# Kernel optimization log

Hardware: AMD Instinct MI355X
Metric: run time of the kernel (lower is better)

## Reference

```python
import jax, jax.numpy as jnp
import numpy as np

B = 131072
SD, AD, HID = 24, 8, 32
NH = SD + AD            # n_heads = 32
UNITS = HID * NH        # 1024


def _xavier(k, shape):
    fan_in, fan_out = shape[-2], shape[-1]
    lim = float(np.sqrt(6.0 / (fan_in + fan_out)))
    return jax.random.uniform(k, shape, jnp.float32, -lim, lim)


def setup_inputs() -> dict:
    key = jax.random.key(0)
    ks = jax.random.split(key, 8)
    return dict(
        state=jax.random.normal(ks[0], (B, SD), jnp.float32),
        action=jax.random.normal(ks[1], (B, AD), jnp.float32),
        # ripple layer 1: per-head Linear(NH -> HID), gate logits init 0 (init_prob=0.5)
        W1=_xavier(ks[2], (NH, NH, HID)), b1=jnp.zeros((NH, HID), jnp.float32), g1=jnp.zeros((NH,), jnp.float32),
        # ripple layer 2: per-head Linear(UNITS -> HID)
        W2=_xavier(ks[3], (NH, UNITS, HID)), b2=jnp.zeros((NH, HID), jnp.float32), g2=jnp.zeros((NH,), jnp.float32),
        # q_network
        Wq1=_xavier(ks[4], (UNITS, 256)), bq1=jnp.zeros((256,), jnp.float32),
        ln1_g=jnp.ones((256,), jnp.float32), ln1_b=jnp.zeros((256,), jnp.float32),
        Wq2=_xavier(ks[5], (256, 128)), bq2=jnp.zeros((128,), jnp.float32),
        ln2_g=jnp.ones((128,), jnp.float32), ln2_b=jnp.zeros((128,), jnp.float32),
        Wq3=_xavier(ks[6], (128, 1)), bq3=jnp.zeros((1,), jnp.float32),
    )


def _ripple(x, W, b, g):
    # x: [B, D]; W: [H, D, K]; per-head linear + tanh, scaled by per-head sigmoid gate
    h = jnp.tanh(jnp.einsum('bd,hdk->bhk', x, W) + b[None])  # [B, H, K]
    h = h * jax.nn.sigmoid(g)[None, :, None]
    return h.reshape(x.shape[0], -1)  # [B, H*K]


def _ln(x, g, b, eps=1e-5):
    mu = jnp.mean(x, -1, keepdims=True)
    var = jnp.mean((x - mu) ** 2, -1, keepdims=True)
    return (x - mu) * jax.lax.rsqrt(var + eps) * g + b


def reference(state, action, W1, b1, g1, W2, b2, g2,
              Wq1, bq1, ln1_g, ln1_b, Wq2, bq2, ln2_g, ln2_b, Wq3, bq3):
    sa = jnp.concatenate([state, action], axis=1)          # [B, SD+AD]
    x = _ripple(sa, W1, b1, g1)                            # [B, UNITS]
    x = _ripple(x, W2, b2, g2)                             # [B, UNITS]
    h = jax.nn.relu(_ln(x @ Wq1 + bq1, ln1_g, ln1_b))      # [B, 256] (dropout = eval identity)
    h = jax.nn.relu(_ln(h @ Wq2 + bq2, ln2_g, ln2_b))      # [B, 128]
    return h @ Wq3 + bq3                                   # [B, 1]
```

## Files before the change

kernel.cpp:

```cpp
#include <hip/hip_runtime.h>
#include <hip/hip_bf16.h>

typedef _Float16 f16x8 __attribute__((ext_vector_type(8)));
typedef _Float16 f16x4 __attribute__((ext_vector_type(4)));
typedef float f32x4 __attribute__((ext_vector_type(4)));

__device__ __forceinline__ float tanh_fast(float x) {
  float e = __expf(2.0f * x);
  return 1.0f - 2.0f * __builtin_amdgcn_rcpf(e + 1.0f);
}
__device__ __forceinline__ float sigmoid_fast(float x) {
  return __builtin_amdgcn_rcpf(1.0f + __expf(-x));
}

__global__ __launch_bounds__(256) void prep_weights(
    const float* __restrict__ W1, const float* __restrict__ W2,
    const float* __restrict__ Wq1, const float* __restrict__ Wq2,
    _Float16* __restrict__ V1p, _Float16* __restrict__ V2p,
    _Float16* __restrict__ T1p, _Float16* __restrict__ T2p) {
  __shared__ float S[32 * 33];
  int b = blockIdx.x, t = threadIdx.x;
  if (b < 2624) {
    const float* in; _Float16* out; int N, nc0, tile, use_pi;
    if (b < 2048) {
      int h = b >> 6, rem = b & 63, ntl = rem >> 5, kt = rem & 31;
      in = W2 + (size_t)h * 32768 + (size_t)kt * 32 * 32;
      N = 32; nc0 = ntl * 16;
      out = V2p; tile = kt * 64 + (h * 2 + ntl); use_pi = 1;
    } else if (b < 2560) {
      int i = b - 2048, nt = i >> 5, kt = i & 31;
      in = Wq1 + (size_t)kt * 32 * 256; N = 256; nc0 = nt * 16;
      out = T1p; tile = kt * 16 + nt; use_pi = 1;
    } else {
      int i = b - 2560, nt = i >> 3, kt = i & 7;
      in = Wq2 + (size_t)kt * 32 * 128; N = 128; nc0 = nt * 16;
      out = T2p; tile = nt * 8 + kt; use_pi = 0;
    }
    if (t < 128) {
      int r = t >> 2, c4 = (t & 3) * 4;
      const float4 v = *(const float4*)(in + (size_t)r * N + nc0 + c4);
      S[r * 17 + c4 + 0] = v.x; S[r * 17 + c4 + 1] = v.y;
      S[r * 17 + c4 + 2] = v.z; S[r * 17 + c4 + 3] = v.w;
    }
    __syncthreads();
    if (t < 128) {
      int w2 = t >> 6, l = t & 63, q = l >> 4, l15 = l & 15;
      f16x4 o;
#pragma unroll
      for (int jj = 0; jj < 4; ++jj) {
        int kl = use_pi ? (q * 4 + jj + w2 * 16) : (q * 8 + w2 * 4 + jj);
        o[jj] = (_Float16)S[kl * 17 + l15];
      }
      *(f16x4*)(out + (size_t)tile * 512 + l * 8 + w2 * 4) = o;
    }
  } else {
    int h = b - 2624;
    const float* in = W1 + h * 1024;
    int cc = t & 31, rr8 = t >> 5;
#pragma unroll
    for (int p = 0; p < 4; ++p) {
      int r = rr8 + p * 8;
      S[cc * 33 + r] = in[r * 32 + cc];
    }
    __syncthreads();
    if (t < 128) {
      int ntl = t >> 6, l = t & 63, q = l >> 4, l15 = l & 15;
      f16x8 o;
#pragma unroll
      for (int j = 0; j < 8; ++j)
        o[j] = (_Float16)S[(ntl * 16 + l15) * 33 + q * 8 + j];
      *(f16x8*)(V1p + (size_t)(h * 2 + ntl) * 512 + l * 8) = o;
    }
  }
}

__global__ __launch_bounds__(256, 2) void k12_fused(
    const float* __restrict__ state, const float* __restrict__ action,
    const _Float16* __restrict__ v1p, const float* __restrict__ b1,
    const float* __restrict__ g1,
    const _Float16* __restrict__ v2p, const float* __restrict__ b2,
    const float* __restrict__ g2,
    _Float16* __restrict__ x2p, int gro, int NRT) {
  __shared__ __align__(16) _Float16 SA[128 * 40];
  __shared__ __align__(16) _Float16 XF[2 * 16384];
  int g = blockIdx.x;
  int bn2 = g & 3, bm = g >> 2;
  int t = threadIdx.x, w = t >> 6, l = t & 63, q = l >> 4, l15 = l & 15;
  int wrow = w & 1, cg2 = w >> 1;
  int m0 = bm * 128;

  {
    int r = t >> 1, half = t & 1;
    size_t grow = (size_t)(gro + m0 + r);
    float v[16];
    if (half == 0) {
      const float4* sp = (const float4*)(state + grow * 24);
      ((float4*)v)[0] = sp[0]; ((float4*)v)[1] = sp[1];
      ((float4*)v)[2] = sp[2]; ((float4*)v)[3] = sp[3];
    } else {
      const float4* sp = (const float4*)(state + grow * 24 + 16);
      ((float4*)v)[0] = sp[0]; ((float4*)v)[1] = sp[1];
      const float4* ap = (const float4*)(action + grow * 8);
      ((float4*)v)[2] = ap[0]; ((float4*)v)[3] = ap[1];
    }
    f16x8 h0, h1;
#pragma unroll
    for (int j = 0; j < 8; ++j) { h0[j] = (_Float16)v[j]; h1[j] = (_Float16)v[8 + j]; }
    *(f16x8*)&SA[r * 40 + half * 16] = h0;
    *(f16x8*)&SA[r * 40 + half * 16 + 8] = h1;
  }
  __syncthreads();

  f16x8 asa[4];
#pragma unroll
  for (int p = 0; p < 4; ++p)
    asa[p] = *(const f16x8*)&SA[((wrow * 4 + p) * 16 + l15) * 40 + q * 8];

  const int nt0 = bn2 * 16 + cg2 * 8;
  const _Float16* bBase = v2p + (size_t)nt0 * 512 + (size_t)l * 8;
  f32x4 acc[4][8] = {};

  auto Rphase = [&](int kcn) {
#pragma unroll
    for (int e = 0; e < 2; ++e) {
      f16x8 rb0 = *(const f16x8*)(v1p + (size_t)(kcn * 8 + cg2 * 4 + 2 * e) * 512 + l * 8);
      f16x8 rb1 = *(const f16x8*)(v1p + (size_t)(kcn * 8 + cg2 * 4 + 2 * e + 1) * 512 + l * 8);
      float sg = sigmoid_fast(g1[kcn * 4 + cg2 * 2 + e]);
      const float* bp = b1 + kcn * 128 + cg2 * 64 + e * 32 + q * 4;
      f32x4 bs0 = *(const f32x4*)(bp);
      f32x4 bs1 = *(const f32x4*)(bp + 16);
      _Float16* bw = XF + ((kcn & 1) * 16384);
#pragma unroll
      for (int p = 0; p < 4; ++p) {
        f32x4 d0 = {}, d1 = {};
        d0 = __builtin_amdgcn_mfma_f32_16x16x32_f16(rb0, asa[p], d0, 0, 0, 0);
        d1 = __builtin_amdgcn_mfma_f32_16x16x32_f16(rb1, asa[p], d1, 0, 0, 0);
        f16x8 o;
#pragma unroll
        for (int r = 0; r < 4; ++r) {
          o[r]     = (_Float16)(tanh_fast(d0[r] + bs0[r]) * sg);
          o[4 + r] = (_Float16)(tanh_fast(d1[r] + bs1[r]) * sg);
        }
        *(f16x8*)(bw + (size_t)((2 * cg2 + e) * 8 + wrow * 4 + p) * 512 + l * 8) = o;
      }
    }
  };

  f16x8 bb0[4], bb1v[4];
#pragma unroll
  for (int n2 = 0; n2 < 4; ++n2)
    bb0[n2] = *(const f16x8*)(bBase + (size_t)n2 * 512);
#pragma unroll
  for (int n2 = 0; n2 < 4; ++n2)
    bb1v[n2] = *(const f16x8*)(bBase + (size_t)(4 + n2) * 512);
  Rphase(0);
  __syncthreads();

#pragma unroll
  for (int kc = 0; kc < 8; ++kc) {
    const _Float16* buf = XF + ((kc & 1) * 16384);
#pragma unroll
    for (int j = 0; j < 4; ++j) {
      if (j == 2 && kc < 7) Rphase(kc + 1);
      int kt = kc * 4 + j;
      f16x8 xa[4];
#pragma unroll
      for (int mi = 0; mi < 4; ++mi)
        xa[mi] = *(const f16x8*)(buf + (size_t)(j * 8 + wrow * 4 + mi) * 512 + l * 8);
#pragma unroll
      for (int mi = 0; mi < 4; ++mi)
#pragma unroll
        for (int n2 = 0; n2 < 4; ++n2)
          acc[mi][n2] = __builtin_amdgcn_mfma_f32_16x16x32_f16(bb0[n2], xa[mi], acc[mi][n2], 0, 0, 0);
      if (kt < 31) {
#pragma unroll
        for (int n2 = 0; n2 < 4; ++n2)
          bb0[n2] = *(const f16x8*)(bBase + (size_t)((kt + 1) * 64 + n2) * 512);
      }
#pragma unroll
      for (int mi = 0; mi < 4; ++mi)
#pragma unroll
        for (int n2 = 0; n2 < 4; ++n2)
          acc[mi][4 + n2] = __builtin_amdgcn_mfma_f32_16x16x32_f16(bb1v[n2], xa[mi], acc[mi][4 + n2], 0, 0, 0);
      if (kt < 31) {
#pragma unroll
        for (int n2 = 0; n2 < 4; ++n2)
          bb1v[n2] = *(const f16x8*)(bBase + (size_t)((kt + 1) * 64 + 4 + n2) * 512);
      }
    }
    __syncthreads();
  }

#pragma unroll
  for (int mi = 0; mi < 4; ++mi) {
    int rt = bm * 8 + wrow * 4 + mi;
#pragma unroll
    for (int p2 = 0; p2 < 4; ++p2) {
      int kc2 = (nt0 >> 1) + p2;
      float sg2 = sigmoid_fast(g2[kc2]);
      f32x4 c0 = *(const f32x4*)(b2 + kc2 * 32 + q * 4);
      f32x4 c1 = *(const f32x4*)(b2 + kc2 * 32 + 16 + q * 4);
      f16x8 o;
#pragma unroll
      for (int r = 0; r < 4; ++r) {
        o[r]     = (_Float16)(tanh_fast(acc[mi][2 * p2][r] + c0[r]) * sg2);
        o[4 + r] = (_Float16)(tanh_fast(acc[mi][2 * p2 + 1][r] + c1[r]) * sg2);
      }
      *(f16x8*)(x2p + ((size_t)kc2 * NRT + rt) * 512 + l * 8) = o;
    }
  }
}

__global__ __launch_bounds__(512, 3) void k3_head(
    const _Float16* __restrict__ x2p, const _Float16* __restrict__ t1p,
    const _Float16* __restrict__ t2p,
    const float* __restrict__ bq1, const float* __restrict__ ln1g, const float* __restrict__ ln1b,
    const float* __restrict__ bq2, const float* __restrict__ ln2g, const float* __restrict__ ln2b,
    const float* __restrict__ wq3, const float* __restrict__ bq3,
    float* __restrict__ out, int NRT, int SROWS) {
  __shared__ __align__(16) _Float16 y1h[128 * 264];
  __shared__ float redA[128 * 4], redB[128 * 4];
  __shared__ float meanv[128], rstdv[128];
  int bm = blockIdx.x;
  int t = threadIdx.x, w = t >> 6, l = t & 63, q = l >> 4, l15 = l & 15;
  int wr = w >> 2, wc = w & 3;

  int gt = bm * 8;
  int slice = 0;
  if (gt >= NRT) { slice = 1; gt -= NRT; }
  int rt0 = gt + wr * 4;

  f32x4 acc[4][4] = {};
  const size_t aStep = (size_t)NRT * 512;
  const _Float16* aP = x2p + (size_t)slice * SROWS * 1024 + (size_t)rt0 * 512 + (size_t)l * 8;
  const _Float16* bP = t1p + (size_t)(wc * 4) * 512 + (size_t)l * 8;

  f16x8 a0[4], a1[4], b0[4], b1[4];
#pragma unroll
  for (int mi = 0; mi < 4; ++mi) a0[mi] = *(const f16x8*)(aP + mi * 512);
#pragma unroll
  for (int ni = 0; ni < 4; ++ni) b0[ni] = *(const f16x8*)(bP + ni * 512);
#pragma unroll
  for (int mi = 0; mi < 4; ++mi) a1[mi] = *(const f16x8*)(aP + aStep + mi * 512);
#pragma unroll
  for (int ni = 0; ni < 4; ++ni) b1[ni] = *(const f16x8*)(bP + 8192 + ni * 512);
  aP += 2 * aStep; bP += 16384;

  for (int kt = 0; kt < 32; kt += 2) {
#pragma unroll
    for (int mi = 0; mi < 4; ++mi)
#pragma unroll
      for (int ni = 0; ni < 4; ++ni)
        acc[mi][ni] = __builtin_amdgcn_mfma_f32_16x16x32_f16(a0[mi], b0[ni], acc[mi][ni], 0, 0, 0);
    if (kt < 30) {
#pragma unroll
      for (int mi = 0; mi < 4; ++mi) a0[mi] = *(const f16x8*)(aP + mi * 512);
#pragma unroll
      for (int ni = 0; ni < 4; ++ni) b0[ni] = *(const f16x8*)(bP + ni * 512);
    }
#pragma unroll
    for (int mi = 0; mi < 4; ++mi)
#pragma unroll
      for (int ni = 0; ni < 4; ++ni)
        acc[mi][ni] = __builtin_amdgcn_mfma_f32_16x16x32_f16(a1[mi], b1[ni], acc[mi][ni], 0, 0, 0);
    if (kt < 30) {
#pragma unroll
      for (int mi = 0; mi < 4; ++mi) a1[mi] = *(const f16x8*)(aP + aStep + mi * 512);
#pragma unroll
      for (int ni = 0; ni < 4; ++ni) b1[ni] = *(const f16x8*)(bP + 8192 + ni * 512);
      aP += 2 * aStep; bP += 16384;
    }
  }

#pragma unroll
  for (int ni = 0; ni < 4; ++ni) {
    int col = wc * 64 + ni * 16 + l15;
    float b = bq1[col];
#pragma unroll
    for (int mi = 0; mi < 4; ++mi)
#pragma unroll
      for (int r = 0; r < 4; ++r) acc[mi][ni][r] += b;
  }
#pragma unroll
  for (int mi = 0; mi < 4; ++mi)
#pragma unroll
    for (int r = 0; r < 4; ++r) {
      int row = wr * 64 + mi * 16 + q * 4 + r;
      float s = 0.f, sq = 0.f;
#pragma unroll
      for (int ni = 0; ni < 4; ++ni) { float v = acc[mi][ni][r]; s += v; sq += v * v; }
#pragma unroll
      for (int off = 1; off < 16; off <<= 1) { s += __shfl_xor(s, off); sq += __shfl_xor(sq, off); }
      if (l15 == 0) { redA[row * 4 + wc] = s; redB[row * 4 + wc] = sq; }
    }
  __syncthreads();
  if (t < 128) {
    float s  = redA[t * 4] + redA[t * 4 + 1] + redA[t * 4 + 2] + redA[t * 4 + 3];
    float sq = redB[t * 4] + redB[t * 4 + 1] + redB[t * 4 + 2] + redB[t * 4 + 3];
    float mean = s * (1.0f / 256.0f);
    float var = sq * (1.0f / 256.0f) - mean * mean;
    meanv[t] = mean; rstdv[t] = rsqrtf(var + 1e-5f);
  }
  __syncthreads();
#pragma unroll
  for (int mi = 0; mi < 4; ++mi)
#pragma unroll
    for (int ni = 0; ni < 4; ++ni)
#pragma unroll
      for (int r = 0; r < 4; ++r) {
        int row = wr * 64 + mi * 16 + q * 4 + r;
        int col = wc * 64 + ni * 16 + l15;
        float y = (acc[mi][ni][r] - meanv[row]) * rstdv[row] * ln1g[col] + ln1b[col];
        y = fmaxf(y, 0.f);
        y1h[row * 264 + col] = (_Float16)y;
      }
  __syncthreads();

  f32x4 a2[4][2] = {};
  for (int kt = 0; kt < 8; ++kt) {
    f16x8 af2[4];
#pragma unroll
    for (int mi = 0; mi < 4; ++mi)
      af2[mi] = *(const f16x8*)&y1h[(wr * 64 + mi * 16 + l15) * 264 + kt * 32 + q * 8];
#pragma unroll
    for (int ni = 0; ni < 2; ++ni) {
      f16x8 bf = *(const f16x8*)(t2p + (size_t)(wc * 2 + ni) * 4096 + kt * 512 + l * 8);
#pragma unroll
      for (int mi = 0; mi < 4; ++mi)
        a2[mi][ni] = __builtin_amdgcn_mfma_f32_16x16x32_f16(af2[mi], bf, a2[mi][ni], 0, 0, 0);
    }
  }
#pragma unroll
  for (int ni = 0; ni < 2; ++ni) {
    int col = wc * 32 + ni * 16 + l15;
    float b = bq2[col];
#pragma unroll
    for (int mi = 0; mi < 4; ++mi)
#pragma unroll
      for (int r = 0; r < 4; ++r) a2[mi][ni][r] += b;
  }
  __syncthreads();
#pragma unroll
  for (int mi = 0; mi < 4; ++mi)
#pragma unroll
    for (int r = 0; r < 4; ++r) {
      int row = wr * 64 + mi * 16 + q * 4 + r;
      float s = 0.f, sq = 0.f;
#pragma unroll
      for (int ni = 0; ni < 2; ++ni) { float v = a2[mi][ni][r]; s += v; sq += v * v; }
#pragma unroll
      for (int off = 1; off < 16; off <<= 1) { s += __shfl_xor(s, off); sq += __shfl_xor(sq, off); }
      if (l15 == 0) { redA[row * 4 + wc] = s; redB[row * 4 + wc] = sq; }
    }
  __syncthreads();
  if (t < 128) {
    float s  = redA[t * 4] + redA[t * 4 + 1] + redA[t * 4 + 2] + redA[t * 4 + 3];
    float sq = redB[t * 4] + redB[t * 4 + 1] + redB[t * 4 + 2] + redB[t * 4 + 3];
    float mean = s * (1.0f / 128.0f);
    float var = sq * (1.0f / 128.0f) - mean * mean;
    meanv[t] = mean; rstdv[t] = rsqrtf(var + 1e-5f);
  }
  __syncthreads();
#pragma unroll
  for (int mi = 0; mi < 4; ++mi)
#pragma unroll
    for (int r = 0; r < 4; ++r) {
      int row = wr * 64 + mi * 16 + q * 4 + r;
      float pr = 0.f;
#pragma unroll
      for (int ni = 0; ni < 2; ++ni) {
        int col = wc * 32 + ni * 16 + l15;
        float y = (a2[mi][ni][r] - meanv[row]) * rstdv[row] * ln2g[col] + ln2b[col];
        y = fmaxf(y, 0.f);
        pr += y * wq3[col];
      }
#pragma unroll
      for (int off = 1; off < 16; off <<= 1) pr += __shfl_xor(pr, off);
      if (l15 == 0) redA[row * 4 + wc] = pr;
    }
  __syncthreads();
  if (t < 128)
    out[bm * 128 + t] = redA[t * 4] + redA[t * 4 + 1] + redA[t * 4 + 2] + redA[t * 4 + 3] + bq3[0];
}

extern "C" void kernel_launch(void* const* d_in, const int* in_sizes, int n_in,
                              void* d_out, int out_size, void* d_ws, size_t ws_size,
                              hipStream_t stream) {
  const float* state  = (const float*)d_in[0];
  const float* action = (const float*)d_in[1];
  const float* W1  = (const float*)d_in[2];
  const float* b1  = (const float*)d_in[3];
  const float* g1  = (const float*)d_in[4];
  const float* W2  = (const float*)d_in[5];
  const float* b2  = (const float*)d_in[6];
  const float* g2  = (const float*)d_in[7];
  const float* Wq1 = (const float*)d_in[8];
  const float* bq1 = (const float*)d_in[9];
  const float* ln1g = (const float*)d_in[10];
  const float* ln1b = (const float*)d_in[11];
  const float* Wq2 = (const float*)d_in[12];
  const float* bq2 = (const float*)d_in[13];
  const float* ln2g = (const float*)d_in[14];
  const float* ln2b = (const float*)d_in[15];
  const float* Wq3 = (const float*)d_in[16];
  const float* bq3 = (const float*)d_in[17];
  int B = in_sizes[0] / 24;

  char* ws = (char*)d_ws;
  _Float16* V1p = (_Float16*)(ws);
  _Float16* V2p = (_Float16*)(ws + 65536);
  _Float16* T1p = (_Float16*)(ws + 65536 + 2097152);
  _Float16* T2p = (_Float16*)(ws + 65536 + 2097152 + 524288);
  size_t woff = (65536 + 2097152 + 524288 + 65536 + 4095) & ~(size_t)4095;

  size_t avail = ws_size > woff ? ws_size - woff : 0;
  long rows = (long)(avail / 2048);
  if (rows > 32768) rows = 32768;
  rows &= ~127L;
  if (rows < 128) rows = 128;
  int S = (int)rows;
  _Float16* x2 = (_Float16*)(ws + woff);
  int NRT = S / 16;

  prep_weights<<<2656, 256, 0, stream>>>(W1, W2, Wq1, Wq2, V1p, V2p, T1p, T2p);

  for (int r0 = 0; r0 < B; r0 += S) {
    int Sc = S < (B - r0) ? S : (B - r0);
    int nbm = Sc / 128;
    k12_fused<<<dim3(4 * nbm), 256, 0, stream>>>(state, action, V1p, b1, g1,
                                                 V2p, b2, g2, x2, r0, NRT);
    k3_head<<<dim3(Sc / 128), 512, 0, stream>>>(x2, T1p, T2p, bq1, ln1g, ln1b,
                                                bq2, ln2g, ln2b, Wq3, bq3,
                                                (float*)d_out + r0, NRT, S);
  }
}
```

Before: 622.2 us.

## Split fused ripple kernel into separate ripple1 and ripple2 kernels

The fused kernel that recomputed ripple layer 1 inside each column block is split in two. A standalone kernel writes layer-1 activations to global workspace, and a 512-thread ripple2 GEMM kernel streams them straight from global memory with a three-deep register prefetch, with no LDS and no per-chunk barriers. This removes the 4x redundant layer-1 recompute, the LDS double buffering and the syncs, but adds a global round trip for x1. It also halves the rows per chunk because workspace is now shared with x1.

```diff
diff --git a/kernel.cpp b/kernel.cpp
--- a/kernel.cpp
+++ b/kernel.cpp
@@ -74,121 +74,115 @@
   }
 }
 
-__global__ __launch_bounds__(256, 2) void k12_fused(
+__global__ __launch_bounds__(256) void k1_ripple1(
     const float* __restrict__ state, const float* __restrict__ action,
     const _Float16* __restrict__ v1p, const float* __restrict__ b1,
-    const float* __restrict__ g1,
-    const _Float16* __restrict__ v2p, const float* __restrict__ b2,
-    const float* __restrict__ g2,
-    _Float16* __restrict__ x2p, int gro, int NRT) {
-  __shared__ __align__(16) _Float16 SA[128 * 40];
-  __shared__ __align__(16) _Float16 XF[2 * 16384];
+    const float* __restrict__ g1, _Float16* __restrict__ x1p,
+    int gro, int NRT) {
+  __shared__ __align__(16) _Float16 SA[64 * 40];
+  int bm = blockIdx.x;
+  int t = threadIdx.x, w = t >> 6, l = t & 63, q = l >> 4, l15 = l & 15;
+  {
+    int r = t >> 2, qq = t & 3;
+    size_t grow = (size_t)(gro + bm * 64 + r);
+    const float* src = (qq < 3) ? (state + grow * 24 + qq * 8)
+                                : (action + grow * 8);
+    float4 v0 = ((const float4*)src)[0];
+    float4 v1 = ((const float4*)src)[1];
+    float v[8] = {v0.x, v0.y, v0.z, v0.w, v1.x, v1.y, v1.z, v1.w};
+    f16x8 h;
+#pragma unroll
+    for (int j = 0; j < 8; ++j) h[j] = (_Float16)v[j];
+    *(f16x8*)&SA[r * 40 + qq * 8] = h;
+  }
+  __syncthreads();
+
+  f16x8 asa[4];
+#pragma unroll
+  for (int p = 0; p < 4; ++p)
+    asa[p] = *(const f16x8*)&SA[(p * 16 + l15) * 40 + q * 8];
+
+#pragma unroll
+  for (int i = 0; i < 8; ++i) {
+    int ktL = w * 8 + i;
+    f16x8 rb0 = *(const f16x8*)(v1p + (size_t)(2 * ktL) * 512 + l * 8);
+    f16x8 rb1 = *(const f16x8*)(v1p + (size_t)(2 * ktL + 1) * 512 + l * 8);
+    float sg = sigmoid_fast(g1[ktL]);
+    f32x4 bs0 = *(const f32x4*)(b1 + ktL * 32 + q * 4);
+    f32x4 bs1 = *(const f32x4*)(b1 + ktL * 32 + 16 + q * 4);
+    _Float16* op = x1p + ((size_t)ktL * NRT + bm * 4) * 512 + l * 8;
+#pragma unroll
+    for (int p = 0; p < 4; ++p) {
+      f32x4 d0 = {}, d1 = {};
+      d0 = __builtin_amdgcn_mfma_f32_16x16x32_f16(rb0, asa[p], d0, 0, 0, 0);
+      d1 = __builtin_amdgcn_mfma_f32_16x16x32_f16(rb1, asa[p], d1, 0, 0, 0);
+      f16x8 o;
+#pragma unroll
+      for (int r = 0; r < 4; ++r) {
+        o[r]     = (_Float16)(tanh_fast(d0[r] + bs0[r]) * sg);
+        o[4 + r] = (_Float16)(tanh_fast(d1[r] + bs1[r]) * sg);
+      }
+      *(f16x8*)(op + (size_t)p * 512) = o;
+    }
+  }
+}
+
+__global__ __launch_bounds__(512, 2) void k2_ripple2(
+    const _Float16* __restrict__ x1p, const _Float16* __restrict__ v2p,
+    const float* __restrict__ b2, const float* __restrict__ g2,
+    _Float16* __restrict__ x2p, int NRT) {
   int g = blockIdx.x;
-  int bn2 = g & 3, bm = g >> 2;
+  int bn = g & 1, bm = g >> 1;
   int t = threadIdx.x, w = t >> 6, l = t & 63, q = l >> 4, l15 = l & 15;
-  int wrow = w & 1, cg2 = w >> 1;
-  int m0 = bm * 128;
-
-  {
-    int r = t >> 1, half = t & 1;
-    size_t grow = (size_t)(gro + m0 + r);
-    float v[16];
-    if (half == 0) {
-      const float4* sp = (const float4*)(state + grow * 24);
-      ((float4*)v)[0] = sp[0]; ((float4*)v)[1] = sp[1];
-      ((float4*)v)[2] = sp[2]; ((float4*)v)[3] = sp[3];
-    } else {
-      const float4* sp = (const float4*)(state + grow * 24 + 16);
-      ((float4*)v)[0] = sp[0]; ((float4*)v)[1] = sp[1];
-      const float4* ap = (const float4*)(action + grow * 8);
-      ((float4*)v)[2] = ap[0]; ((float4*)v)[3] = ap[1];
-    }
-    f16x8 h0, h1;
-#pragma unroll
-    for (int j = 0; j < 8; ++j) { h0[j] = (_Float16)v[j]; h1[j] = (_Float16)v[8 + j]; }
-    *(f16x8*)&SA[r * 40 + half * 16] = h0;
-    *(f16x8*)&SA[r * 40 + half * 16 + 8] = h1;
-  }
-  __syncthreads();
-
-  f16x8 asa[4];
-#pragma unroll
-  for (int p = 0; p < 4; ++p)
-    asa[p] = *(const f16x8*)&SA[((wrow * 4 + p) * 16 + l15) * 40 + q * 8];
-
-  const int nt0 = bn2 * 16 + cg2 * 8;
+  int wrow = w >> 2, wcol = w & 3;
+  const int nt0 = bn * 32 + wcol * 8;
   const _Float16* bBase = v2p + (size_t)nt0 * 512 + (size_t)l * 8;
+  const _Float16* aBase = x1p + (size_t)(bm * 8 + wrow * 4) * 512 + (size_t)l * 8;
+  const size_t aK = (size_t)NRT * 512;
+
   f32x4 acc[4][8] = {};
-
-  auto Rphase = [&](int kcn) {
-#pragma unroll
-    for (int e = 0; e < 2; ++e) {
-      f16x8 rb0 = *(const f16x8*)(v1p + (size_t)(kcn * 8 + cg2 * 4 + 2 * e) * 512 + l * 8);
-      f16x8 rb1 = *(const f16x8*)(v1p + (size_t)(kcn * 8 + cg2 * 4 + 2 * e + 1) * 512 + l * 8);
-      float sg = sigmoid_fast(g1[kcn * 4 + cg2 * 2 + e]);
-      const float* bp = b1 + kcn * 128 + cg2 * 64 + e * 32 + q * 4;
-      f32x4 bs0 = *(const f32x4*)(bp);
-      f32x4 bs1 = *(const f32x4*)(bp + 16);
-      _Float16* bw = XF + ((kcn & 1) * 16384);
-#pragma unroll
-      for (int p = 0; p < 4; ++p) {
-        f32x4 d0 = {}, d1 = {};
-        d0 = __builtin_amdgcn_mfma_f32_16x16x32_f16(rb0, asa[p], d0, 0, 0, 0);
-        d1 = __builtin_amdgcn_mfma_f32_16x16x32_f16(rb1, asa[p], d1, 0, 0, 0);
-        f16x8 o;
-#pragma unroll
-        for (int r = 0; r < 4; ++r) {
-          o[r]     = (_Float16)(tanh_fast(d0[r] + bs0[r]) * sg);
-          o[4 + r] = (_Float16)(tanh_fast(d1[r] + bs1[r]) * sg);
-        }
-        *(f16x8*)(bw + (size_t)((2 * cg2 + e) * 8 + wrow * 4 + p) * 512 + l * 8) = o;
-      }
-    }
-  };
-
-  f16x8 bb0[4], bb1v[4];
-#pragma unroll
-  for (int n2 = 0; n2 < 4; ++n2)
-    bb0[n2] = *(const f16x8*)(bBase + (size_t)n2 * 512);
-#pragma unroll
-  for (int n2 = 0; n2 < 4; ++n2)
-    bb1v[n2] = *(const f16x8*)(bBase + (size_t)(4 + n2) * 512);
-  Rphase(0);
-  __syncthreads();
-
-#pragma unroll
-  for (int kc = 0; kc < 8; ++kc) {
-    const _Float16* buf = XF + ((kc & 1) * 16384);
-#pragma unroll
-    for (int j = 0; j < 4; ++j) {
-      if (j == 2 && kc < 7) Rphase(kc + 1);
-      int kt = kc * 4 + j;
-      f16x8 xa[4];
+  f16x8 bb0[4], bb1[4];
+  f16x8 xa[3][4];
+
+#pragma unroll
+  for (int mi = 0; mi < 4; ++mi) xa[0][mi] = *(const f16x8*)(aBase + mi * 512);
+#pragma unroll
+  for (int mi = 0; mi < 4; ++mi) xa[1][mi] = *(const f16x8*)(aBase + aK + mi * 512);
+#pragma unroll
+  for (int n2 = 0; n2 < 4; ++n2) bb0[n2] = *(const f16x8*)(bBase + (size_t)n2 * 512);
+#pragma unroll
+  for (int n2 = 0; n2 < 4; ++n2) bb1[n2] = *(const f16x8*)(bBase + (size_t)(4 + n2) * 512);
+
+#pragma unroll
+  for (int kt = 0; kt < 32; ++kt) {
+    if (kt < 30) {
 #pragma unroll
       for (int mi = 0; mi < 4; ++mi)
-        xa[mi] = *(const f16x8*)(buf + (size_t)(j * 8 + wrow * 4 + mi) * 512 + l * 8);
-#pragma unroll
-      for (int mi = 0; mi < 4; ++mi)
-#pragma unroll
-        for (int n2 = 0; n2 < 4; ++n2)
-          acc[mi][n2] = __builtin_amdgcn_mfma_f32_16x16x32_f16(bb0[n2], xa[mi], acc[mi][n2], 0, 0, 0);
-      if (kt < 31) {
-#pragma unroll
-        for (int n2 = 0; n2 < 4; ++n2)
-          bb0[n2] = *(const f16x8*)(bBase + (size_t)((kt + 1) * 64 + n2) * 512);
-      }
-#pragma unroll
-      for (int mi = 0; mi < 4; ++mi)
-#pragma unroll
-        for (int n2 = 0; n2 < 4; ++n2)
-          acc[mi][4 + n2] = __builtin_amdgcn_mfma_f32_16x16x32_f16(bb1v[n2], xa[mi], acc[mi][4 + n2], 0, 0, 0);
-      if (kt < 31) {
-#pragma unroll
-        for (int n2 = 0; n2 < 4; ++n2)
-          bb1v[n2] = *(const f16x8*)(bBase + (size_t)((kt + 1) * 64 + 4 + n2) * 512);
-      }
-    }
-    __syncthreads();
+        xa[(kt + 2) % 3][mi] =
+            *(const f16x8*)(aBase + (size_t)(kt + 2) * aK + mi * 512);
+    }
+#pragma unroll
+    for (int mi = 0; mi < 4; ++mi)
+#pragma unroll
+      for (int n2 = 0; n2 < 4; ++n2)
+        acc[mi][n2] = __builtin_amdgcn_mfma_f32_16x16x32_f16(
+            bb0[n2], xa[kt % 3][mi], acc[mi][n2], 0, 0, 0);
+    if (kt < 31) {
+#pragma unroll
+      for (int n2 = 0; n2 < 4; ++n2)
+        bb0[n2] = *(const f16x8*)(bBase + (size_t)((kt + 1) * 64 + n2) * 512);
+    }
+#pragma unroll
+    for (int mi = 0; mi < 4; ++mi)
+#pragma unroll
+      for (int n2 = 0; n2 < 4; ++n2)
+        acc[mi][4 + n2] = __builtin_amdgcn_mfma_f32_16x16x32_f16(
+            bb1[n2], xa[kt % 3][mi], acc[mi][4 + n2], 0, 0, 0);
+    if (kt < 31) {
+#pragma unroll
+      for (int n2 = 0; n2 < 4; ++n2)
+        bb1[n2] = *(const f16x8*)(bBase + (size_t)((kt + 1) * 64 + 4 + n2) * 512);
+    }
   }
 
 #pragma unroll
@@ -414,12 +408,13 @@
   size_t woff = (65536 + 2097152 + 524288 + 65536 + 4095) & ~(size_t)4095;
 
   size_t avail = ws_size > woff ? ws_size - woff : 0;
-  long rows = (long)(avail / 2048);
+  long rows = (long)(avail / 4096);
   if (rows > 32768) rows = 32768;
   rows &= ~127L;
   if (rows < 128) rows = 128;
   int S = (int)rows;
   _Float16* x2 = (_Float16*)(ws + woff);
+  _Float16* x1 = (_Float16*)(ws + woff + (size_t)S * 2048);
   int NRT = S / 16;
 
   prep_weights<<<2656, 256, 0, stream>>>(W1, W2, Wq1, Wq2, V1p, V2p, T1p, T2p);
@@ -427,10 +422,11 @@
   for (int r0 = 0; r0 < B; r0 += S) {
     int Sc = S < (B - r0) ? S : (B - r0);
     int nbm = Sc / 128;
-    k12_fused<<<dim3(4 * nbm), 256, 0, stream>>>(state, action, V1p, b1, g1,
-                                                 V2p, b2, g2, x2, r0, NRT);
-    k3_head<<<dim3(Sc / 128), 512, 0, stream>>>(x2, T1p, T2p, bq1, ln1g, ln1b,
-                                                bq2, ln2g, ln2b, Wq3, bq3,
-                                                (float*)d_out + r0, NRT, S);
-  }
-}
+    k1_ripple1<<<dim3(Sc / 64), 256, 0, stream>>>(state, action, V1p, b1, g1,
+                                                  x1, r0, NRT);
+    k2_ripple2<<<dim3(2 * nbm), 512, 0, stream>>>(x1, V2p, b2, g2, x2, NRT);
+    k3_head<<<dim3(nbm), 512, 0, stream>>>(x2, T1p, T2p, bq1, ln1g, ln1b,
+                                           bq2, ln2g, ln2b, Wq3, bq3,
+                                           (float*)d_out + r0, NRT, S);
+  }
+}
```

Measured after the change: 694.6 us. +11.6%, slower.

## Retile fused ripple kernel to 64-row blocks with half-width column split

Applied to the files above, without the earlier changes.

Changes the k12_fused block tile from 128 rows by a quarter of the layer-2 output columns to 64 rows by half of the columns. Each wave now owns all 64 rows and 8 column tiles, and each wave computes one layer-1 head per phase. This halves the shared-memory footprint and cuts the redundant layer-1 recomputation across column blocks from four copies to two. In exchange each layer-2 weight fragment is reused over fewer rows, so weight traffic per row grows. The grid doubles in size to cover the smaller row tiles.

```diff
diff --git a/kernel.cpp b/kernel.cpp
--- a/kernel.cpp
+++ b/kernel.cpp
@@ -81,68 +81,58 @@
     const _Float16* __restrict__ v2p, const float* __restrict__ b2,
     const float* __restrict__ g2,
     _Float16* __restrict__ x2p, int gro, int NRT) {
-  __shared__ __align__(16) _Float16 SA[128 * 40];
-  __shared__ __align__(16) _Float16 XF[2 * 16384];
+  __shared__ __align__(16) _Float16 SA[64 * 40];
+  __shared__ __align__(16) _Float16 XF[2 * 8192];
   int g = blockIdx.x;
-  int bn2 = g & 3, bm = g >> 2;
+  int bn = g & 1, bm = g >> 1;
   int t = threadIdx.x, w = t >> 6, l = t & 63, q = l >> 4, l15 = l & 15;
-  int wrow = w & 1, cg2 = w >> 1;
-  int m0 = bm * 128;
+  int wcol = w;
+  int m0 = bm * 64;
 
   {
-    int r = t >> 1, half = t & 1;
+    int r = t >> 2, qq = t & 3;
     size_t grow = (size_t)(gro + m0 + r);
-    float v[16];
-    if (half == 0) {
-      const float4* sp = (const float4*)(state + grow * 24);
-      ((float4*)v)[0] = sp[0]; ((float4*)v)[1] = sp[1];
-      ((float4*)v)[2] = sp[2]; ((float4*)v)[3] = sp[3];
-    } else {
-      const float4* sp = (const float4*)(state + grow * 24 + 16);
-      ((float4*)v)[0] = sp[0]; ((float4*)v)[1] = sp[1];
-      const float4* ap = (const float4*)(action + grow * 8);
-      ((float4*)v)[2] = ap[0]; ((float4*)v)[3] = ap[1];
-    }
-    f16x8 h0, h1;
-#pragma unroll
-    for (int j = 0; j < 8; ++j) { h0[j] = (_Float16)v[j]; h1[j] = (_Float16)v[8 + j]; }
-    *(f16x8*)&SA[r * 40 + half * 16] = h0;
-    *(f16x8*)&SA[r * 40 + half * 16 + 8] = h1;
+    const float* src = (qq < 3) ? (state + grow * 24 + qq * 8)
+                                : (action + grow * 8);
+    float4 v0 = ((const float4*)src)[0];
+    float4 v1 = ((const float4*)src)[1];
+    float v[8] = {v0.x, v0.y, v0.z, v0.w, v1.x, v1.y, v1.z, v1.w};
+    f16x8 h;
+#pragma unroll
+    for (int j = 0; j < 8; ++j) h[j] = (_Float16)v[j];
+    *(f16x8*)&SA[r * 40 + qq * 8] = h;
   }
   __syncthreads();
 
   f16x8 asa[4];
 #pragma unroll
   for (int p = 0; p < 4; ++p)
-    asa[p] = *(const f16x8*)&SA[((wrow * 4 + p) * 16 + l15) * 40 + q * 8];
-
-  const int nt0 = bn2 * 16 + cg2 * 8;
+    asa[p] = *(const f16x8*)&SA[(p * 16 + l15) * 40 + q * 8];
+
+  const int nt0 = bn * 32 + wcol * 8;
   const _Float16* bBase = v2p + (size_t)nt0 * 512 + (size_t)l * 8;
   f32x4 acc[4][8] = {};
 
   auto Rphase = [&](int kcn) {
-#pragma unroll
-    for (int e = 0; e < 2; ++e) {
-      f16x8 rb0 = *(const f16x8*)(v1p + (size_t)(kcn * 8 + cg2 * 4 + 2 * e) * 512 + l * 8);
-      f16x8 rb1 = *(const f16x8*)(v1p + (size_t)(kcn * 8 + cg2 * 4 + 2 * e + 1) * 512 + l * 8);
-      float sg = sigmoid_fast(g1[kcn * 4 + cg2 * 2 + e]);
-      const float* bp = b1 + kcn * 128 + cg2 * 64 + e * 32 + q * 4;
-      f32x4 bs0 = *(const f32x4*)(bp);
-      f32x4 bs1 = *(const f32x4*)(bp + 16);
-      _Float16* bw = XF + ((kcn & 1) * 16384);
-#pragma unroll
-      for (int p = 0; p < 4; ++p) {
-        f32x4 d0 = {}, d1 = {};
-        d0 = __builtin_amdgcn_mfma_f32_16x16x32_f16(rb0, asa[p], d0, 0, 0, 0);
-        d1 = __builtin_amdgcn_mfma_f32_16x16x32_f16(rb1, asa[p], d1, 0, 0, 0);
-        f16x8 o;
-#pragma unroll
-        for (int r = 0; r < 4; ++r) {
-          o[r]     = (_Float16)(tanh_fast(d0[r] + bs0[r]) * sg);
-          o[4 + r] = (_Float16)(tanh_fast(d1[r] + bs1[r]) * sg);
-        }
-        *(f16x8*)(bw + (size_t)((2 * cg2 + e) * 8 + wrow * 4 + p) * 512 + l * 8) = o;
-      }
+    int ktL = kcn * 4 + wcol;
+    f16x8 rb0 = *(const f16x8*)(v1p + (size_t)(2 * ktL) * 512 + l * 8);
+    f16x8 rb1 = *(const f16x8*)(v1p + (size_t)(2 * ktL + 1) * 512 + l * 8);
+    float sg = sigmoid_fast(g1[ktL]);
+    f32x4 bs0 = *(const f32x4*)(b1 + ktL * 32 + q * 4);
+    f32x4 bs1 = *(const f32x4*)(b1 + ktL * 32 + 16 + q * 4);
+    _Float16* bw = XF + ((kcn & 1) * 8192);
+#pragma unroll
+    for (int p = 0; p < 4; ++p) {
+      f32x4 d0 = {}, d1 = {};
+      d0 = __builtin_amdgcn_mfma_f32_16x16x32_f16(rb0, asa[p], d0, 0, 0, 0);
+      d1 = __builtin_amdgcn_mfma_f32_16x16x32_f16(rb1, asa[p], d1, 0, 0, 0);
+      f16x8 o;
+#pragma unroll
+      for (int r = 0; r < 4; ++r) {
+        o[r]     = (_Float16)(tanh_fast(d0[r] + bs0[r]) * sg);
+        o[4 + r] = (_Float16)(tanh_fast(d1[r] + bs1[r]) * sg);
+      }
+      *(f16x8*)(bw + (size_t)(wcol * 4 + p) * 512 + l * 8) = o;
     }
   };
 
@@ -158,7 +148,7 @@
 
 #pragma unroll
   for (int kc = 0; kc < 8; ++kc) {
-    const _Float16* buf = XF + ((kc & 1) * 16384);
+    const _Float16* buf = XF + ((kc & 1) * 8192);
 #pragma unroll
     for (int j = 0; j < 4; ++j) {
       if (j == 2 && kc < 7) Rphase(kc + 1);
@@ -166,7 +156,7 @@
       f16x8 xa[4];
 #pragma unroll
       for (int mi = 0; mi < 4; ++mi)
-        xa[mi] = *(const f16x8*)(buf + (size_t)(j * 8 + wrow * 4 + mi) * 512 + l * 8);
+        xa[mi] = *(const f16x8*)(buf + (size_t)(j * 4 + mi) * 512 + l * 8);
 #pragma unroll
       for (int mi = 0; mi < 4; ++mi)
 #pragma unroll
@@ -193,7 +183,7 @@
 
 #pragma unroll
   for (int mi = 0; mi < 4; ++mi) {
-    int rt = bm * 8 + wrow * 4 + mi;
+    int rt = bm * 4 + mi;
 #pragma unroll
     for (int p2 = 0; p2 < 4; ++p2) {
       int kc2 = (nt0 >> 1) + p2;
@@ -427,10 +417,10 @@
   for (int r0 = 0; r0 < B; r0 += S) {
     int Sc = S < (B - r0) ? S : (B - r0);
     int nbm = Sc / 128;
-    k12_fused<<<dim3(4 * nbm), 256, 0, stream>>>(state, action, V1p, b1, g1,
-                                                 V2p, b2, g2, x2, r0, NRT);
-    k3_head<<<dim3(Sc / 128), 512, 0, stream>>>(x2, T1p, T2p, bq1, ln1g, ln1b,
-                                                bq2, ln2g, ln2b, Wq3, bq3,
-                                                (float*)d_out + r0, NRT, S);
-  }
-}
+    k12_fused<<<dim3(2 * (Sc / 64)), 256, 0, stream>>>(state, action, V1p, b1, g1,
+                                                       V2p, b2, g2, x2, r0, NRT);
+    k3_head<<<dim3(nbm), 512, 0, stream>>>(x2, T1p, T2p, bq1, ln1g, ln1b,
+                                           bq2, ln2g, ln2b, Wq3, bq3,
+                                           (float*)d_out + r0, NRT, S);
+  }
+}
```

Result: slower. 641.3 us (+3.1%).
